# Kernel optimization log

Measured on AMD Instinct MI355X. Metric: run time of the kernel, lower is better.

## Reference

```python
import jax, jax.numpy as jnp
import numpy as np

N_NODES = 50000
N_EDGES = 800000
HIDDEN = 128
BN_EPS = 1e-5


def setup_inputs() -> dict:
    key = jax.random.key(0)
    ks = jax.random.split(key, 4)
    x = jax.random.normal(ks[0], (N_NODES, HIDDEN), dtype=jnp.float32)
    edge_index = jax.random.randint(ks[1], (2, N_EDGES), 0, N_NODES, dtype=jnp.int64)
    scale = 1.0 / np.sqrt(HIDDEN)
    W1 = jax.random.normal(ks[2], (HIDDEN, HIDDEN), dtype=jnp.float32) * scale
    b1 = jnp.zeros((HIDDEN,), dtype=jnp.float32)
    W2 = jax.random.normal(ks[3], (HIDDEN, HIDDEN), dtype=jnp.float32) * scale
    b2 = jnp.zeros((HIDDEN,), dtype=jnp.float32)
    gamma = jnp.ones((HIDDEN,), dtype=jnp.float32)
    beta = jnp.zeros((HIDDEN,), dtype=jnp.float32)
    return {"x": x, "edge_index": edge_index, "W1": W1, "b1": b1,
            "W2": W2, "b2": b2, "gamma": gamma, "beta": beta}


def reference(x, edge_index, W1, b1, W2, b2, gamma, beta):
    # GINConv (eps=0): h_i = MLP( x_i + sum_{(j->i) in E} x_j )
    src = edge_index[0]
    dst = edge_index[1]
    agg = jax.ops.segment_sum(x[src], dst, num_segments=x.shape[0])  # [N, H]
    h = x + agg
    # 2-layer MLP: Linear -> ReLU -> Linear
    h = jnp.maximum(h @ W1 + b1, 0.0)
    h = h @ W2 + b2
    # BatchNorm1d over node dimension (training-mode batch statistics)
    mean = jnp.mean(h, axis=0)
    var = jnp.var(h, axis=0)
    h = (h - mean) * jax.lax.rsqrt(var + BN_EPS) * gamma + beta
    # add_activation=False (default): no ReLU. Dropout in eval mode: identity.
    return h
```

## Files before the change

kernel.cpp:

```cpp
#include <hip/hip_runtime.h>

typedef unsigned int u32;
typedef unsigned short u16;
typedef __attribute__((ext_vector_type(8))) short short8;
typedef __attribute__((ext_vector_type(4))) float f32x4;

static constexpr int NN = 50000;
static constexpr int NE = 800000;
static constexpr int HH = 128;
static constexpr int NB1 = (NN + 1023) / 1024;
static constexpr int NBK = 196;
static constexpr int EPB = 8192;
static constexpr int NEB = (NE + EPB - 1) / EPB;

__device__ __forceinline__ u32 bf16r(float f) {
  u32 u = __builtin_bit_cast(u32, f);
  return (u + 0x7FFFu + ((u >> 16) & 1u)) >> 16;
}
__device__ __forceinline__ u32 pk2(float lo, float hi) { return bf16r(lo) | (bf16r(hi) << 16); }
__device__ __forceinline__ float bl(u32 p) { return __builtin_bit_cast(float, p << 16); }
__device__ __forceinline__ float bh(u32 p) { return __builtin_bit_cast(float, p & 0xFFFF0000u); }

__global__ __launch_bounds__(256) void prep_kernel(const float4* __restrict__ x,
                                                   uint4* __restrict__ x16,
                                                   const float* __restrict__ W1,
                                                   u16* __restrict__ w1t,
                                                   const float* __restrict__ W2,
                                                   u16* __restrict__ w2t,
                                                   float* __restrict__ stats,
                                                   const int* __restrict__ ei,
                                                   int* __restrict__ hist2d) {
  __shared__ int hist[NBK];
  const int b = blockIdx.x, t = threadIdx.x;
  if (b < 3125) {
    const int i = b * 256 + t;
    const float4 a = x[2 * i];
    const float4 c = x[2 * i + 1];
    uint4 o;
    o.x = pk2(a.x, a.y);
    o.y = pk2(a.z, a.w);
    o.z = pk2(c.x, c.y);
    o.w = pk2(c.z, c.w);
    x16[i] = o;
  } else if (b < 3189) {
    const int o = (b - 3125) * 256 + t;
    const int n = o >> 7, k = o & 127;
    w1t[o] = (u16)bf16r(W1[k * 128 + n]);
  } else if (b < 3253) {
    const int o = (b - 3189) * 256 + t;
    const int n = o >> 7, k = o & 127;
    w2t[o] = (u16)bf16r(W2[k * 128 + n]);
  } else if (b == 3253) {
    stats[t] = 0.f;
  } else {
    const int hb = b - 3254;
    for (int i = t; i < NBK; i += 256) hist[i] = 0;
    __syncthreads();
    const int e0 = hb * EPB;
    const int e1 = min(e0 + EPB, NE);
    for (int e = e0 + t; e < e1; e += 256) atomicAdd(&hist[ei[NE + e] >> 8], 1);
    __syncthreads();
    for (int i = t; i < NBK; i += 256) hist2d[hb * NBK + i] = hist[i];
  }
}

__global__ __launch_bounds__(256) void ph3_kernel(const int* __restrict__ ei,
                                                  const int* __restrict__ hist2d,
                                                  u32* __restrict__ packed) {
  __shared__ int cur[NBK];
  __shared__ int tot[256];
  const int b = blockIdx.x, t = threadIdx.x;
  int total = 0, partial = 0;
  if (t < NBK) {
    for (int bb = 0; bb < NEB; ++bb) {
      const int v = hist2d[bb * NBK + t];
      total += v;
      if (bb < b) partial += v;
    }
  }
  tot[t] = total;
  __syncthreads();
  for (int off = 1; off < 256; off <<= 1) {
    const int add = (t >= off) ? tot[t - off] : 0;
    __syncthreads();
    tot[t] += add;
    __syncthreads();
  }
  if (t < NBK) cur[t] = (t ? tot[t - 1] : 0) + partial;
  __syncthreads();
  const int e0 = b * EPB;
  const int e1 = min(e0 + EPB, NE);
  for (int e = e0 + t; e < e1; e += 256) {
    const int s = ei[e];
    const int d = ei[NE + e];
    const int pos = atomicAdd(&cur[d >> 8], 1);
    packed[pos] = (u32)s | ((u32)(d & 255) << 16);
  }
}

__global__ __launch_bounds__(256) void ph4_kernel(const int* __restrict__ hist2d,
                                                  const u32* __restrict__ packed,
                                                  int* __restrict__ offs,
                                                  int* __restrict__ srcl) {
  __shared__ int hist[256];
  __shared__ int scn[256];
  __shared__ int sb[2];
  const int b = blockIdx.x, t = threadIdx.x;
  int total = 0;
  if (t < NBK)
    for (int bb = 0; bb < NEB; ++bb) total += hist2d[bb * NBK + t];
  scn[t] = total;
  __syncthreads();
  for (int off = 1; off < 256; off <<= 1) {
    const int add = (t >= off) ? scn[t - off] : 0;
    __syncthreads();
    scn[t] += add;
    __syncthreads();
  }
  if (t == b) {
    sb[0] = b ? scn[b - 1] : 0;
    sb[1] = scn[b];
  }
  __syncthreads();
  const int base = sb[0];
  const int cnt = sb[1] - base;

  hist[t] = 0;
  __syncthreads();
  for (int i = t; i < cnt; i += 256) atomicAdd(&hist[packed[base + i] >> 16], 1);
  __syncthreads();
  scn[t] = hist[t];
  __syncthreads();
  for (int off = 1; off < 256; off <<= 1) {
    const int add = (t >= off) ? scn[t - off] : 0;
    __syncthreads();
    scn[t] += add;
    __syncthreads();
  }
  const int excl = t ? scn[t - 1] : 0;
  const int node = b * 256 + t;
  if (node < NN) offs[node] = base + excl;
  if (b == NBK - 1 && t == 0) offs[NN] = NE;
  __syncthreads();
  hist[t] = excl;
  __syncthreads();
  for (int i = t; i < cnt; i += 256) {
    const u32 p = packed[base + i];
    const int r = atomicAdd(&hist[p >> 16], 1);
    srcl[base + r] = (int)(p & 0xFFFFu);
  }
}

__global__ __launch_bounds__(256) void gmlp_kernel(const u32* __restrict__ x16,
                                                   const int* __restrict__ offs,
                                                   const int* __restrict__ srcl,
                                                   const u16* __restrict__ w1t,
                                                   const float* __restrict__ b1,
                                                   const u16* __restrict__ w2t,
                                                   const float* __restrict__ b2,
                                                   u32* __restrict__ h2,
                                                   float* __restrict__ stats,
                                                   int nchunk) {
  __shared__ __align__(16) u16 hs0[16][136];
  __shared__ __align__(16) u16 hs1[16][136];
  __shared__ float sstats[256];
  const int t = threadIdx.x;
  const int w = t >> 6;
  const int lane = t & 63;
  const int lhi = lane >> 4, llo = lane & 15;
  const int q = t >> 4, l16 = t & 15;
  sstats[t] = 0.f;

  short8 w1f[2][4], w2f[2][4];
  float4 bs1[2], bs2[2];
#pragma unroll
  for (int c = 0; c < 2; ++c) {
    const int ct = 2 * w + c;
#pragma unroll
    for (int kb = 0; kb < 4; ++kb) {
      w1f[c][kb] = *reinterpret_cast<const short8*>(w1t + (size_t)(16 * ct + llo) * 128 + kb * 32 + lhi * 8);
      w2f[c][kb] = *reinterpret_cast<const short8*>(w2t + (size_t)(16 * ct + llo) * 128 + kb * 32 + lhi * 8);
    }
    bs1[c] = *reinterpret_cast<const float4*>(b1 + ct * 16 + lhi * 4);
    bs2[c] = *reinterpret_cast<const float4*>(b2 + ct * 16 + lhi * 4);
  }
  __syncthreads();

  for (int ch = blockIdx.x; ch < nchunk; ch += gridDim.x) {
    const int row0 = ch * 16;

    {
      const int node = row0 + q;
      const uint4 sv = reinterpret_cast<const uint4*>(x16 + (size_t)node * 64)[l16];
      float a0 = bl(sv.x), a1 = bh(sv.x), a2 = bl(sv.y), a3 = bh(sv.y);
      float a4 = bl(sv.z), a5 = bh(sv.z), a6 = bl(sv.w), a7 = bh(sv.w);
      const int beg = offs[node], end = offs[node + 1];
      int e = beg;
      for (; e + 8 <= end; e += 8) {
        int s[8];
#pragma unroll
        for (int j = 0; j < 8; ++j) s[j] = srcl[e + j];
        uint4 v[8];
#pragma unroll
        for (int j = 0; j < 8; ++j)
          v[j] = reinterpret_cast<const uint4*>(x16 + (size_t)s[j] * 64)[l16];
#pragma unroll
        for (int j = 0; j < 8; ++j) {
          a0 += bl(v[j].x); a1 += bh(v[j].x);
          a2 += bl(v[j].y); a3 += bh(v[j].y);
          a4 += bl(v[j].z); a5 += bh(v[j].z);
          a6 += bl(v[j].w); a7 += bh(v[j].w);
        }
      }
      for (; e < end; ++e) {
        const uint4 v = reinterpret_cast<const uint4*>(x16 + (size_t)srcl[e] * 64)[l16];
        a0 += bl(v.x); a1 += bh(v.x);
        a2 += bl(v.y); a3 += bh(v.y);
        a4 += bl(v.z); a5 += bh(v.z);
        a6 += bl(v.w); a7 += bh(v.w);
      }
      uint4 o;
      o.x = pk2(a0, a1);
      o.y = pk2(a2, a3);
      o.z = pk2(a4, a5);
      o.w = pk2(a6, a7);
      *reinterpret_cast<uint4*>(&hs0[q][l16 * 8]) = o;
    }
    __syncthreads();

    short8 afr[4];
#pragma unroll
    for (int kb = 0; kb < 4; ++kb)
      afr[kb] = *reinterpret_cast<const short8*>(&hs0[llo][kb * 32 + lhi * 8]);

    f32x4 acc0 = {0.f, 0.f, 0.f, 0.f};
    f32x4 acc1 = {0.f, 0.f, 0.f, 0.f};
#pragma unroll
    for (int kb = 0; kb < 4; ++kb) {
      acc0 = __builtin_amdgcn_mfma_f32_16x16x32_bf16(w1f[0][kb], afr[kb], acc0, 0, 0, 0);
      acc1 = __builtin_amdgcn_mfma_f32_16x16x32_bf16(w1f[1][kb], afr[kb], acc1, 0, 0, 0);
    }

#pragma unroll
    for (int c = 0; c < 2; ++c) {
      const int ct = 2 * w + c;
      const f32x4 a = c ? acc1 : acc0;
      const float4 bb = c ? bs1[1] : bs1[0];
      const float v0 = fmaxf(a[0] + bb.x, 0.f);
      const float v1 = fmaxf(a[1] + bb.y, 0.f);
      const float v2 = fmaxf(a[2] + bb.z, 0.f);
      const float v3 = fmaxf(a[3] + bb.w, 0.f);
      u32* dst = reinterpret_cast<u32*>(&hs1[llo][ct * 16 + lhi * 4]);
      dst[0] = pk2(v0, v1);
      dst[1] = pk2(v2, v3);
    }
    __syncthreads();

    short8 af2[4];
#pragma unroll
    for (int kb = 0; kb < 4; ++kb)
      af2[kb] = *reinterpret_cast<const short8*>(&hs1[llo][kb * 32 + lhi * 8]);

    f32x4 dcc0 = {0.f, 0.f, 0.f, 0.f};
    f32x4 dcc1 = {0.f, 0.f, 0.f, 0.f};
#pragma unroll
    for (int kb = 0; kb < 4; ++kb) {
      dcc0 = __builtin_amdgcn_mfma_f32_16x16x32_bf16(w2f[0][kb], af2[kb], dcc0, 0, 0, 0);
      dcc1 = __builtin_amdgcn_mfma_f32_16x16x32_bf16(w2f[1][kb], af2[kb], dcc1, 0, 0, 0);
    }

#pragma unroll
    for (int c = 0; c < 2; ++c) {
      const int ct = 2 * w + c;
      const f32x4 a = c ? dcc1 : dcc0;
      const float4 bb = c ? bs2[1] : bs2[0];
      float v0 = a[0] + bb.x;
      float v1 = a[1] + bb.y;
      float v2 = a[2] + bb.z;
      float v3 = a[3] + bb.w;
      u32* op = h2 + (size_t)(row0 + llo) * 64 + ct * 8 + lhi * 2;
      op[0] = pk2(v0, v1);
      op[1] = pk2(v2, v3);
      float q0 = v0 * v0, q1 = v1 * v1, q2 = v2 * v2, q3 = v3 * v3;
#pragma unroll
      for (int m = 1; m < 16; m <<= 1) {
        v0 += __shfl_xor(v0, m, 64); v1 += __shfl_xor(v1, m, 64);
        v2 += __shfl_xor(v2, m, 64); v3 += __shfl_xor(v3, m, 64);
        q0 += __shfl_xor(q0, m, 64); q1 += __shfl_xor(q1, m, 64);
        q2 += __shfl_xor(q2, m, 64); q3 += __shfl_xor(q3, m, 64);
      }
      if (llo == 0) {
        const int cb = ct * 16 + lhi * 4;
        atomicAdd(&sstats[cb + 0], v0); atomicAdd(&sstats[cb + 1], v1);
        atomicAdd(&sstats[cb + 2], v2); atomicAdd(&sstats[cb + 3], v3);
        atomicAdd(&sstats[128 + cb + 0], q0); atomicAdd(&sstats[128 + cb + 1], q1);
        atomicAdd(&sstats[128 + cb + 2], q2); atomicAdd(&sstats[128 + cb + 3], q3);
      }
    }
  }
  __syncthreads();
  atomicAdd(&stats[t], sstats[t]);
}

__global__ __launch_bounds__(256) void bn16_kernel(const u32* __restrict__ h2,
                                                   const float* __restrict__ stats,
                                                   const float* __restrict__ gamma,
                                                   const float* __restrict__ beta,
                                                   float* __restrict__ out, float invn) {
  __shared__ float scale_s[128], shift_s[128];
  const int t = threadIdx.x;
  if (t < 128) {
    const float mean = stats[t] * invn;
    float var = fmaf(-mean, mean, stats[128 + t] * invn);
    var = fmaxf(var, 0.f);
    const float rs = rsqrtf(var + 1e-5f);
    const float sc = gamma[t] * rs;
    scale_s[t] = sc;
    shift_s[t] = fmaf(-mean, sc, beta[t]);
  }
  __syncthreads();
  int i = blockIdx.x * 256 + t;
  const int stride = gridDim.x * 256;
  for (; i < NN * 64; i += stride) {
    const int c = (i & 63) * 2;
    const u32 p = h2[i];
    float2 o;
    o.x = fmaf(bl(p), scale_s[c + 0], shift_s[c + 0]);
    o.y = fmaf(bh(p), scale_s[c + 1], shift_s[c + 1]);
    *reinterpret_cast<float2*>(out + 2 * (size_t)i) = o;
  }
}

__global__ void zero_stats_kernel(float* __restrict__ stats) { stats[threadIdx.x] = 0.f; }

__global__ __launch_bounds__(256) void zero_int_kernel(int* __restrict__ p, int n) {
  int i = blockIdx.x * blockDim.x + threadIdx.x;
  const int stride = gridDim.x * blockDim.x;
  for (; i < n; i += stride) p[i] = 0;
}

__global__ __launch_bounds__(256) void count_kernel(const int* __restrict__ ei,
                                                    int* __restrict__ cnt) {
  const int e = blockIdx.x * blockDim.x + threadIdx.x;
  if (e < NE) atomicAdd(&cnt[ei[NE + e]], 1);
}

__global__ __launch_bounds__(256) void scan1_kernel(const int* __restrict__ cnt,
                                                    int* __restrict__ offs,
                                                    int* __restrict__ partials) {
  __shared__ int tsum[256];
  const int b = blockIdx.x, t = threadIdx.x;
  const int base = b * 1024 + t * 4;
  int v[4];
  int s = 0;
#pragma unroll
  for (int j = 0; j < 4; ++j) {
    const int idx = base + j;
    v[j] = (idx < NN) ? cnt[idx] : 0;
    s += v[j];
  }
  tsum[t] = s;
  __syncthreads();
#pragma unroll
  for (int off = 1; off < 256; off <<= 1) {
    const int add = (t >= off) ? tsum[t - off] : 0;
    __syncthreads();
    tsum[t] += add;
    __syncthreads();
  }
  int excl = (t ? tsum[t - 1] : 0);
#pragma unroll
  for (int j = 0; j < 4; ++j) {
    const int idx = base + j;
    if (idx < NN) offs[idx] = excl;
    excl += v[j];
  }
  if (t == 255) partials[b] = tsum[255];
}

__global__ void scan2_kernel(int* __restrict__ partials, int nb) {
  const int t = threadIdx.x;
  int v = (t < nb) ? partials[t] : 0;
#pragma unroll
  for (int off = 1; off < 64; off <<= 1) {
    const int n = __shfl_up(v, off, 64);
    if (t >= off) v += n;
  }
  int excl = __shfl_up(v, 1, 64);
  if (t == 0) excl = 0;
  if (t < nb) partials[t] = excl;
}

__global__ __launch_bounds__(256) void scan3_kernel(int* __restrict__ offs,
                                                    int* __restrict__ cursor,
                                                    const int* __restrict__ partials) {
  const int b = blockIdx.x;
  const int add = partials[b];
#pragma unroll
  for (int j = 0; j < 4; ++j) {
    const int idx = b * 1024 + threadIdx.x + j * 256;
    if (idx < NN) {
      const int o = offs[idx] + add;
      offs[idx] = o;
      cursor[idx] = o;
    }
  }
  if (b == 0 && threadIdx.x == 0) offs[NN] = NE;
}

__global__ __launch_bounds__(256) void fill_kernel(const int* __restrict__ ei,
                                                   int* __restrict__ cursor,
                                                   int* __restrict__ srcl) {
  const int e = blockIdx.x * blockDim.x + threadIdx.x;
  if (e >= NE) return;
  const int s = ei[e];
  const int d = ei[NE + e];
  const int pos = atomicAdd(&cursor[d], 1);
  srcl[pos] = s;
}

__global__ __launch_bounds__(256) void gather_kernel(const float* __restrict__ x,
                                                     const int* __restrict__ offs,
                                                     const int* __restrict__ srcl,
                                                     float* __restrict__ out) {
  const int wave = (blockIdx.x * 256 + threadIdx.x) >> 6;
  const int lane = threadIdx.x & 63;
  const int nwaves = gridDim.x * 4;
  for (int node = wave; node < NN; node += nwaves) {
    float2 acc = *reinterpret_cast<const float2*>(x + (size_t)node * HH + lane * 2);
    const int beg = offs[node], end = offs[node + 1];
    for (int e = beg; e < end; ++e) {
      const int s = srcl[e];
      const float2 v = *reinterpret_cast<const float2*>(x + (size_t)s * HH + lane * 2);
      acc.x += v.x;
      acc.y += v.y;
    }
    *reinterpret_cast<float2*>(out + (size_t)node * HH + lane * 2) = acc;
  }
}

__global__ __launch_bounds__(256) void copy_x_kernel(const float4* __restrict__ x,
                                                     float4* __restrict__ h, int n4) {
  int i = blockIdx.x * blockDim.x + threadIdx.x;
  const int stride = gridDim.x * blockDim.x;
  for (; i < n4; i += stride) h[i] = x[i];
}

__global__ __launch_bounds__(256) void scatter_kernel(const float* __restrict__ x,
                                                      const int* __restrict__ ei,
                                                      float* __restrict__ h) {
  const long long tid = (long long)blockIdx.x * blockDim.x + threadIdx.x;
  const int e = (int)(tid >> 5);
  if (e >= NE) return;
  const int c = (int)(tid & 31);
  const int s = ei[e];
  const int d = ei[NE + e];
  const float4 v = *reinterpret_cast<const float4*>(x + (size_t)s * HH + c * 4);
  float* dp = h + (size_t)d * HH + c * 4;
  atomicAdd(dp + 0, v.x);
  atomicAdd(dp + 1, v.y);
  atomicAdd(dp + 2, v.z);
  atomicAdd(dp + 3, v.w);
}

template <bool RELU>
__global__ __launch_bounds__(256, 2) void gemm128_kernel(const float* in,
                                                         const float* __restrict__ W,
                                                         const float* __restrict__ bias,
                                                         float* out,
                                                         int nrows, int nchunks) {
  __shared__ float Ws[128][128];
  __shared__ float rows_s[32][128];
  const int t = threadIdx.x;
  for (int i = t; i < 128 * 128 / 4; i += 256) {
    reinterpret_cast<float4*>(&Ws[0][0])[i] = reinterpret_cast<const float4*>(W)[i];
  }
  const int col4 = (t & 31) * 4;
  const int rowg = (t >> 5) * 4;
  const float4 b4 = *reinterpret_cast<const float4*>(bias + col4);

  for (int chunk = blockIdx.x; chunk < nchunks; chunk += gridDim.x) {
    const int row0 = chunk * 32;
    __syncthreads();
    for (int i = t; i < 1024; i += 256) {
      const int rr = i >> 5, cc = (i & 31) * 4;
      const int grow = row0 + rr;
      float4 v = make_float4(0.f, 0.f, 0.f, 0.f);
      if (grow < nrows) v = *reinterpret_cast<const float4*>(in + (size_t)grow * HH + cc);
      *reinterpret_cast<float4*>(&rows_s[rr][cc]) = v;
    }
    __syncthreads();

    float acc[4][4] = {};
#pragma unroll 4
    for (int k = 0; k < 128; k += 4) {
      float4 a[4];
#pragma unroll
      for (int r = 0; r < 4; ++r) a[r] = *reinterpret_cast<const float4*>(&rows_s[rowg + r][k]);
#pragma unroll
      for (int kk = 0; kk < 4; ++kk) {
        const float4 wv = *reinterpret_cast<const float4*>(&Ws[k + kk][col4]);
#pragma unroll
        for (int r = 0; r < 4; ++r) {
          const float av = (&a[r].x)[kk];
          acc[r][0] = fmaf(av, wv.x, acc[r][0]);
          acc[r][1] = fmaf(av, wv.y, acc[r][1]);
          acc[r][2] = fmaf(av, wv.z, acc[r][2]);
          acc[r][3] = fmaf(av, wv.w, acc[r][3]);
        }
      }
    }

#pragma unroll
    for (int r = 0; r < 4; ++r) {
      const int grow = row0 + rowg + r;
      if (grow < nrows) {
        float4 o;
        o.x = acc[r][0] + b4.x;
        o.y = acc[r][1] + b4.y;
        o.z = acc[r][2] + b4.z;
        o.w = acc[r][3] + b4.w;
        if (RELU) {
          o.x = fmaxf(o.x, 0.f); o.y = fmaxf(o.y, 0.f);
          o.z = fmaxf(o.z, 0.f); o.w = fmaxf(o.w, 0.f);
        }
        *reinterpret_cast<float4*>(out + (size_t)grow * HH + col4) = o;
      }
    }
  }
}

__global__ __launch_bounds__(256) void col_stats_kernel(const float* __restrict__ h,
                                                        float* __restrict__ stats, int nrows) {
  __shared__ float ssum[256], ssq[256];
  const int t = threadIdx.x;
  const int col = t & 127;
  const int half = t >> 7;
  float s = 0.f, q = 0.f;
  for (int r = blockIdx.x * 2 + half; r < nrows; r += gridDim.x * 2) {
    const float v = h[(size_t)r * HH + col];
    s += v;
    q = fmaf(v, v, q);
  }
  ssum[t] = s;
  ssq[t] = q;
  __syncthreads();
  if (t < 128) {
    atomicAdd(&stats[col], ssum[t] + ssum[t + 128]);
    atomicAdd(&stats[128 + col], ssq[t] + ssq[t + 128]);
  }
}

__global__ __launch_bounds__(256) void bn_apply_kernel(float* __restrict__ h,
                                                       const float* __restrict__ stats,
                                                       const float* __restrict__ gamma,
                                                       const float* __restrict__ beta,
                                                       int n4, float invn) {
  __shared__ float scale_s[128], shift_s[128];
  const int t = threadIdx.x;
  if (t < 128) {
    const float mean = stats[t] * invn;
    float var = fmaf(-mean, mean, stats[128 + t] * invn);
    var = fmaxf(var, 0.f);
    const float rs = rsqrtf(var + 1e-5f);
    const float sc = gamma[t] * rs;
    scale_s[t] = sc;
    shift_s[t] = fmaf(-mean, sc, beta[t]);
  }
  __syncthreads();
  float4* h4 = reinterpret_cast<float4*>(h);
  int i = blockIdx.x * blockDim.x + threadIdx.x;
  const int stride = gridDim.x * blockDim.x;
  for (; i < n4; i += stride) {
    const int c = (i & 31) * 4;
    float4 v = h4[i];
    v.x = fmaf(v.x, scale_s[c + 0], shift_s[c + 0]);
    v.y = fmaf(v.y, scale_s[c + 1], shift_s[c + 1]);
    v.z = fmaf(v.z, scale_s[c + 2], shift_s[c + 2]);
    v.w = fmaf(v.w, scale_s[c + 3], shift_s[c + 3]);
    h4[i] = v;
  }
}

extern "C" void kernel_launch(void* const* d_in, const int* in_sizes, int n_in,
                              void* d_out, int out_size, void* d_ws, size_t ws_size,
                              hipStream_t stream) {
  const float* x = (const float*)d_in[0];
  const int* ei = (const int*)d_in[1];
  const float* W1 = (const float*)d_in[2];
  const float* b1 = (const float*)d_in[3];
  const float* W2 = (const float*)d_in[4];
  const float* b2 = (const float*)d_in[5];
  const float* gamma = (const float*)d_in[6];
  const float* beta = (const float*)d_in[7];
  float* out = (float*)d_out;

  auto AL = [](size_t v) { return (v + 255) & ~(size_t)255; };
  const size_t offs_b = AL((size_t)(NN + 1) * 4);
  const size_t srcl_b = AL((size_t)NE * 4);
  const size_t packed_b = AL((size_t)NE * 4);
  const size_t h2d_b = AL((size_t)NEB * NBK * 4);
  const size_t stats_b = AL(256 * 4);
  const size_t x16_b = AL((size_t)NN * HH * 2);
  const size_t h2_b = AL((size_t)NN * HH * 2);
  const size_t wt_b = AL((size_t)128 * 128 * 2);
  const size_t need_A = offs_b + srcl_b + packed_b + h2d_b + stats_b + x16_b + h2_b +
                        2 * wt_b;

  const size_t cnt_b = AL((size_t)NN * 4);
  const size_t part_b = AL(64 * 4);
  const size_t need_B = offs_b + cnt_b + part_b + srcl_b + stats_b;

  if (ws_size >= need_A) {
    char* p = (char*)d_ws;
    int* offs = (int*)p;       p += offs_b;
    int* srcl = (int*)p;       p += srcl_b;
    u32* packed = (u32*)p;     p += packed_b;
    int* hist2d = (int*)p;     p += h2d_b;
    float* stats = (float*)p;  p += stats_b;
    u16* x16 = (u16*)p;        p += x16_b;
    u32* h2 = (u32*)p;         p += h2_b;
    u16* w1t = (u16*)p;        p += wt_b;
    u16* w2t = (u16*)p;

    prep_kernel<<<3254 + NEB, 256, 0, stream>>>((const float4*)x, (uint4*)x16, W1, w1t,
                                                W2, w2t, stats, ei, hist2d);
    ph3_kernel<<<NEB, 256, 0, stream>>>(ei, hist2d, packed);
    ph4_kernel<<<NBK, 256, 0, stream>>>(hist2d, packed, offs, srcl);

    const int nchunk = NN / 16;
    gmlp_kernel<<<1024, 256, 0, stream>>>((const u32*)x16, offs, srcl, w1t, b1, w2t, b2,
                                          h2, stats, nchunk);
    bn16_kernel<<<2048, 256, 0, stream>>>(h2, stats, gamma, beta, out, 1.0f / NN);
  } else if (ws_size >= need_B) {
    char* p = (char*)d_ws;
    int* offs = (int*)p;      p += offs_b;
    int* cnt = (int*)p;       p += cnt_b;
    int* partials = (int*)p;  p += part_b;
    int* srcl = (int*)p;      p += srcl_b;
    float* stats = (float*)p;

    zero_int_kernel<<<64, 256, 0, stream>>>(cnt, NN);
    count_kernel<<<(NE + 255) / 256, 256, 0, stream>>>(ei, cnt);
    scan1_kernel<<<NB1, 256, 0, stream>>>(cnt, offs, partials);
    scan2_kernel<<<1, 64, 0, stream>>>(partials, NB1);
    scan3_kernel<<<NB1, 256, 0, stream>>>(offs, cnt, partials);
    fill_kernel<<<(NE + 255) / 256, 256, 0, stream>>>(ei, cnt, srcl);
    gather_kernel<<<1024, 256, 0, stream>>>(x, offs, srcl, out);

    zero_stats_kernel<<<1, 256, 0, stream>>>(stats);
    const int nchunks = (NN + 31) / 32;
    gemm128_kernel<true><<<512, 256, 0, stream>>>(out, W1, b1, out, NN, nchunks);
    gemm128_kernel<false><<<512, 256, 0, stream>>>(out, W2, b2, out, NN, nchunks);
    col_stats_kernel<<<1024, 256, 0, stream>>>(out, stats, NN);
    bn_apply_kernel<<<2048, 256, 0, stream>>>(out, stats, gamma, beta, NN * HH / 4, 1.0f / NN);
  } else {
    float* stats = (float*)d_ws;
    copy_x_kernel<<<2048, 256, 0, stream>>>((const float4*)x, (float4*)out, NN * HH / 4);
    const long long sthreads = (long long)NE * 32;
    scatter_kernel<<<(int)((sthreads + 255) / 256), 256, 0, stream>>>(x, ei, out);
    zero_stats_kernel<<<1, 256, 0, stream>>>(stats);
    const int nchunks = (NN + 31) / 32;
    gemm128_kernel<true><<<512, 256, 0, stream>>>(out, W1, b1, out, NN, nchunks);
    gemm128_kernel<false><<<512, 256, 0, stream>>>(out, W2, b2, out, NN, nchunks);
    col_stats_kernel<<<1024, 256, 0, stream>>>(out, stats, NN);
    bn_apply_kernel<<<2048, 256, 0, stream>>>(out, stats, gamma, beta, NN * HH / 4, 1.0f / NN);
  }
}
```

Baseline: 145.9 us.

## Split gather from MLP into separate kernels, staging aggregate through output buffer

The neighbour gather-sum moves out of the fused MLP kernel into its own kernel, which writes the bf16 aggregate into the output buffer. The MLP kernel then loads A fragments directly from global memory, and the x16 buffer is reused for h2 to shrink the workspace. The aim is to let the latency-bound gather run at full occupancy without MFMA and barrier stalls, and to run the MLP with fewer blocks. The cost is an extra global write and read of the N×128 bf16 aggregate plus one more kernel launch.

After: 131.5 us. 9.8% less time.

```diff
diff --git a/kernel.cpp b/kernel.cpp
--- a/kernel.cpp
+++ b/kernel.cpp
@@ -151,24 +151,65 @@
   }
 }
 
-__global__ __launch_bounds__(256) void gmlp_kernel(const u32* __restrict__ x16,
-                                                   const int* __restrict__ offs,
-                                                   const int* __restrict__ srcl,
-                                                   const u16* __restrict__ w1t,
-                                                   const float* __restrict__ b1,
-                                                   const u16* __restrict__ w2t,
-                                                   const float* __restrict__ b2,
-                                                   u32* __restrict__ h2,
-                                                   float* __restrict__ stats,
-                                                   int nchunk) {
-  __shared__ __align__(16) u16 hs0[16][136];
-  __shared__ __align__(16) u16 hs1[16][136];
+__global__ __launch_bounds__(256) void gather16_kernel(const u32* __restrict__ x16,
+                                                       const int* __restrict__ offs,
+                                                       const int* __restrict__ srcl,
+                                                       u32* __restrict__ h0) {
+  const int qw = (blockIdx.x * 256 + threadIdx.x) >> 4;
+  const int l16 = threadIdx.x & 15;
+  const int nqw = gridDim.x * 16;
+  const uint4* x4 = reinterpret_cast<const uint4*>(x16);
+  for (int node = qw; node < NN; node += nqw) {
+    const uint4 sv = x4[(size_t)node * 16 + l16];
+    float a0 = bl(sv.x), a1 = bh(sv.x), a2 = bl(sv.y), a3 = bh(sv.y);
+    float a4 = bl(sv.z), a5 = bh(sv.z), a6 = bl(sv.w), a7 = bh(sv.w);
+    const int beg = offs[node], end = offs[node + 1];
+    int e = beg;
+    for (; e + 8 <= end; e += 8) {
+      int s[8];
+#pragma unroll
+      for (int j = 0; j < 8; ++j) s[j] = srcl[e + j];
+      uint4 v[8];
+#pragma unroll
+      for (int j = 0; j < 8; ++j) v[j] = x4[(size_t)s[j] * 16 + l16];
+#pragma unroll
+      for (int j = 0; j < 8; ++j) {
+        a0 += bl(v[j].x); a1 += bh(v[j].x);
+        a2 += bl(v[j].y); a3 += bh(v[j].y);
+        a4 += bl(v[j].z); a5 += bh(v[j].z);
+        a6 += bl(v[j].w); a7 += bh(v[j].w);
+      }
+    }
+    for (; e < end; ++e) {
+      const uint4 v = x4[(size_t)srcl[e] * 16 + l16];
+      a0 += bl(v.x); a1 += bh(v.x);
+      a2 += bl(v.y); a3 += bh(v.y);
+      a4 += bl(v.z); a5 += bh(v.z);
+      a6 += bl(v.w); a7 += bh(v.w);
+    }
+    uint4 o;
+    o.x = pk2(a0, a1);
+    o.y = pk2(a2, a3);
+    o.z = pk2(a4, a5);
+    o.w = pk2(a6, a7);
+    reinterpret_cast<uint4*>(h0)[(size_t)node * 16 + l16] = o;
+  }
+}
+
+__global__ __launch_bounds__(256) void fused_mlp_kernel(const u16* __restrict__ h0,
+                                                        const u16* __restrict__ w1t,
+                                                        const float* __restrict__ b1,
+                                                        const u16* __restrict__ w2t,
+                                                        const float* __restrict__ b2,
+                                                        u32* __restrict__ h2,
+                                                        float* __restrict__ stats,
+                                                        int nchunk) {
+  __shared__ __align__(16) u16 hs[16][136];
   __shared__ float sstats[256];
   const int t = threadIdx.x;
   const int w = t >> 6;
   const int lane = t & 63;
   const int lhi = lane >> 4, llo = lane & 15;
-  const int q = t >> 4, l16 = t & 15;
   sstats[t] = 0.f;
 
   short8 w1f[2][4], w2f[2][4];
@@ -189,49 +230,11 @@
   for (int ch = blockIdx.x; ch < nchunk; ch += gridDim.x) {
     const int row0 = ch * 16;
 
-    {
-      const int node = row0 + q;
-      const uint4 sv = reinterpret_cast<const uint4*>(x16 + (size_t)node * 64)[l16];
-      float a0 = bl(sv.x), a1 = bh(sv.x), a2 = bl(sv.y), a3 = bh(sv.y);
-      float a4 = bl(sv.z), a5 = bh(sv.z), a6 = bl(sv.w), a7 = bh(sv.w);
-      const int beg = offs[node], end = offs[node + 1];
-      int e = beg;
-      for (; e + 8 <= end; e += 8) {
-        int s[8];
-#pragma unroll
-        for (int j = 0; j < 8; ++j) s[j] = srcl[e + j];
-        uint4 v[8];
-#pragma unroll
-        for (int j = 0; j < 8; ++j)
-          v[j] = reinterpret_cast<const uint4*>(x16 + (size_t)s[j] * 64)[l16];
-#pragma unroll
-        for (int j = 0; j < 8; ++j) {
-          a0 += bl(v[j].x); a1 += bh(v[j].x);
-          a2 += bl(v[j].y); a3 += bh(v[j].y);
-          a4 += bl(v[j].z); a5 += bh(v[j].z);
-          a6 += bl(v[j].w); a7 += bh(v[j].w);
-        }
-      }
-      for (; e < end; ++e) {
-        const uint4 v = reinterpret_cast<const uint4*>(x16 + (size_t)srcl[e] * 64)[l16];
-        a0 += bl(v.x); a1 += bh(v.x);
-        a2 += bl(v.y); a3 += bh(v.y);
-        a4 += bl(v.z); a5 += bh(v.z);
-        a6 += bl(v.w); a7 += bh(v.w);
-      }
-      uint4 o;
-      o.x = pk2(a0, a1);
-      o.y = pk2(a2, a3);
-      o.z = pk2(a4, a5);
-      o.w = pk2(a6, a7);
-      *reinterpret_cast<uint4*>(&hs0[q][l16 * 8]) = o;
-    }
-    __syncthreads();
-
+    const u16* arow = h0 + (size_t)(row0 + llo) * 128;
     short8 afr[4];
 #pragma unroll
     for (int kb = 0; kb < 4; ++kb)
-      afr[kb] = *reinterpret_cast<const short8*>(&hs0[llo][kb * 32 + lhi * 8]);
+      afr[kb] = *reinterpret_cast<const short8*>(arow + kb * 32 + lhi * 8);
 
     f32x4 acc0 = {0.f, 0.f, 0.f, 0.f};
     f32x4 acc1 = {0.f, 0.f, 0.f, 0.f};
@@ -250,7 +253,7 @@
       const float v1 = fmaxf(a[1] + bb.y, 0.f);
       const float v2 = fmaxf(a[2] + bb.z, 0.f);
       const float v3 = fmaxf(a[3] + bb.w, 0.f);
-      u32* dst = reinterpret_cast<u32*>(&hs1[llo][ct * 16 + lhi * 4]);
+      u32* dst = reinterpret_cast<u32*>(&hs[llo][ct * 16 + lhi * 4]);
       dst[0] = pk2(v0, v1);
       dst[1] = pk2(v2, v3);
     }
@@ -259,7 +262,7 @@
     short8 af2[4];
 #pragma unroll
     for (int kb = 0; kb < 4; ++kb)
-      af2[kb] = *reinterpret_cast<const short8*>(&hs1[llo][kb * 32 + lhi * 8]);
+      af2[kb] = *reinterpret_cast<const short8*>(&hs[llo][kb * 32 + lhi * 8]);
 
     f32x4 dcc0 = {0.f, 0.f, 0.f, 0.f};
     f32x4 dcc1 = {0.f, 0.f, 0.f, 0.f};
@@ -268,6 +271,7 @@
       dcc0 = __builtin_amdgcn_mfma_f32_16x16x32_bf16(w2f[0][kb], af2[kb], dcc0, 0, 0, 0);
       dcc1 = __builtin_amdgcn_mfma_f32_16x16x32_bf16(w2f[1][kb], af2[kb], dcc1, 0, 0, 0);
     }
+    __syncthreads();
 
 #pragma unroll
     for (int c = 0; c < 2; ++c) {
@@ -602,10 +606,8 @@
   const size_t h2d_b = AL((size_t)NEB * NBK * 4);
   const size_t stats_b = AL(256 * 4);
   const size_t x16_b = AL((size_t)NN * HH * 2);
-  const size_t h2_b = AL((size_t)NN * HH * 2);
   const size_t wt_b = AL((size_t)128 * 128 * 2);
-  const size_t need_A = offs_b + srcl_b + packed_b + h2d_b + stats_b + x16_b + h2_b +
-                        2 * wt_b;
+  const size_t need_A = offs_b + srcl_b + packed_b + h2d_b + stats_b + x16_b + 2 * wt_b;
 
   const size_t cnt_b = AL((size_t)NN * 4);
   const size_t part_b = AL(64 * 4);
@@ -619,7 +621,6 @@
     int* hist2d = (int*)p;     p += h2d_b;
     float* stats = (float*)p;  p += stats_b;
     u16* x16 = (u16*)p;        p += x16_b;
-    u32* h2 = (u32*)p;         p += h2_b;
     u16* w1t = (u16*)p;        p += wt_b;
     u16* w2t = (u16*)p;
 
@@ -628,9 +629,12 @@
     ph3_kernel<<<NEB, 256, 0, stream>>>(ei, hist2d, packed);
     ph4_kernel<<<NBK, 256, 0, stream>>>(hist2d, packed, offs, srcl);
 
+    gather16_kernel<<<2048, 256, 0, stream>>>((const u32*)x16, offs, srcl, (u32*)d_out);
+
     const int nchunk = NN / 16;
-    gmlp_kernel<<<1024, 256, 0, stream>>>((const u32*)x16, offs, srcl, w1t, b1, w2t, b2,
-                                          h2, stats, nchunk);
+    u32* h2 = (u32*)x16;
+    fused_mlp_kernel<<<512, 256, 0, stream>>>((const u16*)d_out, w1t, b1, w2t, b2,
+                                              h2, stats, nchunk);
     bn16_kernel<<<2048, 256, 0, stream>>>(h2, stats, gamma, beta, out, 1.0f / NN);
   } else if (ws_size >= need_B) {
     char* p = (char*)d_ws;
```
